# Kernel tuning notes

Hardware: AMD Instinct MI355X
Metric: run time of the kernel (lower is better)

Reference implementation:

```python
import jax, jax.numpy as jnp
import numpy as np

NH, NKV, HD, ROPE_DIMS, ROPE_BASE = 16, 4, 128, 64, 10000.0


def _rms_norm(x):
    eps = jnp.asarray(jnp.finfo(x.dtype).eps, x.dtype)
    return x * jax.lax.rsqrt(jnp.mean(x * x, axis=-1, keepdims=True) + eps)


def _apply_rope_partial(x, cos, sin):
    # x: [B, H, T, hd]; cos/sin: [T, rope_dims//2]
    h = ROPE_DIMS // 2
    xa, xb, xp = x[..., :h], x[..., h:ROPE_DIMS], x[..., ROPE_DIMS:]
    c, s = cos[None, None], sin[None, None]
    rot = jnp.concatenate([xa * c - xb * s, xa * s + xb * c], axis=-1)
    return jnp.concatenate([rot, xp], axis=-1)


def setup_inputs() -> dict:
    key = jax.random.key(0)
    ks = jax.random.split(key, 7)
    B, T, D = 2, 2048, 2048
    kv_dim = NKV * HD
    sc = lambda n: 1.0 / np.sqrt(n)
    return {
        "x": jax.random.normal(ks[0], (B, T, D), jnp.float32),
        "ve_embed": jax.random.normal(ks[1], (B, T, kv_dim), jnp.float32),
        "Wq": jax.random.normal(ks[2], (D, D), jnp.float32) * sc(D),
        "Wk": jax.random.normal(ks[3], (kv_dim, D), jnp.float32) * sc(D),
        "Wv": jax.random.normal(ks[4], (kv_dim, D), jnp.float32) * sc(D),
        "Wproj": jax.random.normal(ks[5], (D, D), jnp.float32) * sc(D),
        "q_gain": jnp.full((NH,), 12.0, jnp.float32)
        + 0.01 * jax.random.normal(ks[6], (NH,), jnp.float32),
    }


def reference(x, ve_embed, Wq, Wk, Wv, Wproj, q_gain):
    B, T, D = x.shape
    g = NH // NKV  # GQA group size

    # QKV projections -> [B, H, T, hd]
    q = (x @ Wq.T).reshape(B, T, NH, HD).transpose(0, 2, 1, 3)
    k = (x @ Wk.T).reshape(B, T, NKV, HD).transpose(0, 2, 1, 3)
    v = (x @ Wv.T).reshape(B, T, NKV, HD).transpose(0, 2, 1, 3)

    q, k = _rms_norm(q), _rms_norm(k)

    # partial RoPE (frequencies built over full hd, first rope_dims//2 used)
    inv_freq = 1.0 / ROPE_BASE ** (jnp.arange(0, HD, 2, dtype=jnp.float32) / HD)
    f = jnp.arange(T, dtype=jnp.float32)[:, None] * inv_freq[None, :]  # [T, hd//2]
    cos, sin = jnp.cos(f)[:, : ROPE_DIMS // 2], jnp.sin(f)[:, : ROPE_DIMS // 2]
    q = _apply_rope_partial(q, cos, sin)
    k = _apply_rope_partial(k, cos, sin)

    q = q * q_gain[None, :, None, None]
    v = v + ve_embed.reshape(B, T, NKV, HD).transpose(0, 2, 1, 3)

    # GQA causal attention: q grouped as [B, nkv, g, T, hd]
    qg = q.reshape(B, NKV, g, T, HD)
    scale = 1.0 / np.sqrt(HD)
    scores = jnp.einsum("bkgtd,bksd->bkgts", qg, k) * scale
    causal = jnp.tril(jnp.ones((T, T), bool))
    scores = jnp.where(causal[None, None, None], scores, -jnp.inf)
    p = jax.nn.softmax(scores, axis=-1)
    y = jnp.einsum("bkgts,bksd->bkgtd", p, v)  # [B, nkv, g, T, hd]

    y = y.reshape(B, NH, T, HD).transpose(0, 2, 1, 3).reshape(B, T, D)
    return y @ Wproj.T
```

## Files before the change

kernel.cpp:

```cpp
#include <hip/hip_runtime.h>
#include <hip/hip_bf16.h>
#include <cstdint>
#include <cstddef>


typedef _Float16 f16_t;
typedef f16_t f16x8 __attribute__((ext_vector_type(8)));
typedef float f32x4 __attribute__((ext_vector_type(4)));

#define MFMA16F(a, b, c) __builtin_amdgcn_mfma_f32_16x16x32_f16((a), (b), (c), 0, 0, 0)
#define SBAR()   __builtin_amdgcn_s_barrier()
#define SCHED0() __builtin_amdgcn_sched_barrier(0)
#define LGKM0()  asm volatile("s_waitcnt lgkmcnt(0)" ::: "memory")

__device__ __forceinline__ void gload16(const f16_t* g, f16_t* l) {
  auto lds_ptr = reinterpret_cast<__attribute__((address_space(3))) unsigned int*>(
      reinterpret_cast<uintptr_t>(l));
  auto g_ptr = reinterpret_cast<const __attribute__((address_space(1))) unsigned int*>(
      reinterpret_cast<uintptr_t>(g));
  __builtin_amdgcn_global_load_lds(g_ptr, lds_ptr, 16, 0, 0);
}

__global__ void k_cast_f16(const float* __restrict__ in, f16_t* __restrict__ o, long n) {
  long i = ((long)blockIdx.x * blockDim.x + threadIdx.x) * 4;
  const long step = (long)gridDim.x * blockDim.x * 4;
  for (; i < n; i += step) {
    const float4 v = *reinterpret_cast<const float4*>(in + i);
    f16_t r[4] = {(f16_t)v.x, (f16_t)v.y, (f16_t)v.z, (f16_t)v.w};
    *reinterpret_cast<uint64_t*>(o + i) = *reinterpret_cast<const uint64_t*>(r);
  }
}

__global__ void k_cast_wqkv(const float* __restrict__ Wq, const float* __restrict__ Wk,
                            const float* __restrict__ Wv, f16_t* __restrict__ wf) {
  long i = ((long)blockIdx.x * blockDim.x + threadIdx.x) * 4;
  const long step = (long)gridDim.x * blockDim.x * 4;
  for (; i < (long)3072 * 2048; i += step) {
    const long row = i >> 11, col = i & 2047;
    const float* src = (row < 2048) ? (Wq + (size_t)row * 2048)
                     : (row < 2560) ? (Wk + (size_t)(row - 2048) * 2048)
                                    : (Wv + (size_t)(row - 2560) * 2048);
    const float4 v = *reinterpret_cast<const float4*>(src + col);
    f16_t r[4] = {(f16_t)v.x, (f16_t)v.y, (f16_t)v.z, (f16_t)v.w};
    *reinterpret_cast<uint64_t*>(wf + row * 2048 + col) = *reinterpret_cast<const uint64_t*>(r);
  }
}

__global__ void k_rope_tab(float* __restrict__ ctab, float* __restrict__ stab) {
  const int idx = blockIdx.x * blockDim.x + threadIdx.x;
  if (idx >= 2048 * 32) return;
  const int t = idx >> 5, i = idx & 31;
  const float freq = exp2f(-(float)i * 0.2076205059304601f);
  const float f = (float)t * freq;
  ctab[idx] = cosf(f);
  stab[idx] = sinf(f);
}

__global__ __launch_bounds__(256) void k_vtrans(
    const f16_t* __restrict__ vn, f16_t* __restrict__ vt)
{
  __shared__ __align__(16) f16_t lsT[64 * 136];
  const int t0 = blockIdx.x * 64;
  const int bk = blockIdx.y;
  const f16_t* src = vn + ((size_t)bk * 2048 + t0) * 128;
  f16_t* dst = vt + (size_t)bk * 128 * 2048;
  const int tid = threadIdx.x;
#pragma unroll
  for (int it = 0; it < 4; ++it) {
    const int cch = tid + it * 256;
    const int r = cch >> 4, c = cch & 15;
    *reinterpret_cast<f16x8*>(&lsT[r * 136 + c * 8]) =
        *reinterpret_cast<const f16x8*>(src + (size_t)r * 128 + c * 8);
  }
  __syncthreads();
#pragma unroll
  for (int it = 0; it < 4; ++it) {
    const int u = tid + it * 256;
    const int d = u >> 3, c8 = u & 7;
    f16_t vals[8];
#pragma unroll
    for (int j = 0; j < 8; ++j) vals[j] = lsT[(c8 * 8 + j) * 136 + d];
    *reinterpret_cast<f16x8*>(dst + (size_t)d * 2048 + t0 + c8 * 8) =
        *reinterpret_cast<const f16x8*>(vals);
  }
}

template <int NBU, typename OutT>
__global__ __launch_bounds__(1024, 1) void k_gemmQ(
    const f16_t* __restrict__ A, const f16_t* __restrict__ Bm,
    OutT* __restrict__ C, int M, int N, int K, int lda, int ldb)
{
  __shared__ __align__(16) f16_t lds[2][(4 + NBU) * 4096];
  const int tid = threadIdx.x;
  const int l = tid & 63, w = tid >> 6;
  const int lrow = l & 15, lk = l >> 4;
  const int wm = w >> 2, wn = w & 3;

  const int nwg = gridDim.x * gridDim.y;
  int lin = blockIdx.y * gridDim.x + blockIdx.x;
  lin = (lin & 7) * (nwg >> 3) + (lin >> 3);
  const int m0 = (lin / gridDim.x) * 256, n0 = (lin % gridDim.x) * (64 * NBU);

  const bool stager = (tid < 512);
  const int srow = tid >> 3;
  const int scol = ((tid & 7) ^ (srow & 7)) << 3;
  const f16_t* gP[4 + NBU];
#pragma unroll
  for (int u = 0; u < 4; ++u) gP[u] = A + (size_t)(m0 + u * 64 + srow) * lda + scol;
#pragma unroll
  for (int u = 0; u < NBU; ++u) gP[4 + u] = Bm + (size_t)(n0 + u * 64 + srow) * ldb + scol;

  auto stageAll = [&](int buf, int k0) {
#pragma unroll
    for (int u = 0; u < 4 + NBU; ++u)
      gload16(gP[u] + k0, &lds[buf][u * 4096 + tid * 8]);
  };
  auto rdA = [&](int buf, int mf, int ks) -> f16x8 {
    const int row = wm * 64 + mf * 16 + lrow;
    const int slot = ((ks << 2) | lk) ^ (row & 7);
    return *reinterpret_cast<const f16x8*>(&lds[buf][row * 64 + slot * 8]);
  };
  auto rdB = [&](int buf, int nf, int ks) -> f16x8 {
    const int row = wn * (16 * NBU) + nf * 16 + lrow;
    const int slot = ((ks << 2) | lk) ^ (row & 7);
    return *reinterpret_cast<const f16x8*>(&lds[buf][16384 + row * 64 + slot * 8]);
  };

  f32x4 acc[4][NBU] = {};
  const int nkt = K >> 6;

  if (stager) {
    stageAll(0, 0);
    stageAll(1, nkt > 1 ? 64 : 0);
  }
  if constexpr (NBU == 3) { asm volatile("s_waitcnt vmcnt(7)" ::: "memory"); }
  else                    { asm volatile("s_waitcnt vmcnt(6)" ::: "memory"); }
  SCHED0();
  SBAR(); SCHED0();

  f16x8 aA[4][2], bB[NBU][2];
  for (int kt = 0; kt < nkt; ++kt) {
    const int b = kt & 1;
    const int kn2 = (kt + 2 < nkt ? kt + 2 : nkt - 1) << 6;

#pragma unroll
    for (int mf = 0; mf < 4; ++mf) { aA[mf][0] = rdA(b, mf, 0); aA[mf][1] = rdA(b, mf, 1); }
#pragma unroll
    for (int nf = 0; nf < NBU; ++nf) { bB[nf][0] = rdB(b, nf, 0); bB[nf][1] = rdB(b, nf, 1); }
    __builtin_amdgcn_s_setprio(1);
#pragma unroll
    for (int mf = 0; mf < 2; ++mf)
#pragma unroll
      for (int nf = 0; nf < NBU; ++nf)
#pragma unroll
        for (int ks = 0; ks < 2; ++ks)
          acc[mf][nf] = MFMA16F(aA[mf][ks], bB[nf][ks], acc[mf][nf]);
    __builtin_amdgcn_s_setprio(0);
    LGKM0(); SCHED0();
    SBAR(); SCHED0();

    if (stager) stageAll(b, kn2);
    if constexpr (NBU == 3) { asm volatile("s_waitcnt vmcnt(7)" ::: "memory"); }
    else                    { asm volatile("s_waitcnt vmcnt(6)" ::: "memory"); }
    SCHED0();
    __builtin_amdgcn_s_setprio(1);
#pragma unroll
    for (int mf = 2; mf < 4; ++mf)
#pragma unroll
      for (int nf = 0; nf < NBU; ++nf)
#pragma unroll
        for (int ks = 0; ks < 2; ++ks)
          acc[mf][nf] = MFMA16F(aA[mf][ks], bB[nf][ks], acc[mf][nf]);
    __builtin_amdgcn_s_setprio(0);
    SBAR(); SCHED0();
  }

#pragma unroll
  for (int mf = 0; mf < 4; ++mf) {
    const int row = m0 + wm * 64 + mf * 16 + lk * 4;
#pragma unroll
    for (int nf = 0; nf < NBU; ++nf) {
      const int col = n0 + wn * (16 * NBU) + nf * 16 + lrow;
#pragma unroll
      for (int rg = 0; rg < 4; ++rg)
        C[(size_t)(row + rg) * N + col] = (OutT)acc[mf][nf][rg];
    }
  }
  (void)M;
}

__global__ __launch_bounds__(256) void k_qkv_epi(
    const f16_t* __restrict__ qkv, const float* __restrict__ ve,
    const float* __restrict__ qgain,
    const float* __restrict__ ctab, const float* __restrict__ stab,
    f16_t* __restrict__ qn, f16_t* __restrict__ kn, f16_t* __restrict__ vn)
{
  const int blk = blockIdx.x;
  const int b = blk >> 11, t = blk & 2047;
  const int w = threadIdx.x >> 6, l = threadIdx.x & 63;
  const int i32 = l & 31;
  const float c = ctab[t * 32 + i32], s = stab[t * 32 + i32];
  const float EPS = 1.1920929e-07f;
  constexpr float SCALE_L2E = 0.088388347648318447f * 1.4426950408889634f;

#pragma unroll
  for (int it = 0; it < 4; ++it) {
    const int h = w + it * 4;
    const f16_t* row = qkv + (size_t)blk * 3072 + h * 128;
    float x0 = (float)row[l], x1 = (float)row[l + 64];
    float ss = x0 * x0 + x1 * x1;
#pragma unroll
    for (int off = 32; off; off >>= 1) ss += __shfl_xor(ss, off);
    const float rn = rsqrtf(ss * (1.0f / 128.0f) + EPS);
    x0 *= rn; x1 *= rn;
    const float p = __shfl_xor(x0, 32);
    float xr = (l < 32) ? (x0 * c - p * s) : (p * s + x0 * c);
    const float g = qgain[h] * SCALE_L2E;
    xr *= g; x1 *= g;
    f16_t* orow = qn + (((size_t)(b * 16 + h)) * 2048 + t) * 128;
    orow[l] = (f16_t)xr;
    orow[l + 64] = (f16_t)x1;
  }
  {
    const f16_t* row = qkv + (size_t)blk * 3072 + 2048 + w * 128;
    float x0 = (float)row[l], x1 = (float)row[l + 64];
    float ss = x0 * x0 + x1 * x1;
#pragma unroll
    for (int off = 32; off; off >>= 1) ss += __shfl_xor(ss, off);
    const float rn = rsqrtf(ss * (1.0f / 128.0f) + EPS);
    x0 *= rn; x1 *= rn;
    const float p = __shfl_xor(x0, 32);
    const float xr = (l < 32) ? (x0 * c - p * s) : (p * s + x0 * c);
    f16_t* orow = kn + (((size_t)(b * 4 + w)) * 2048 + t) * 128;
    orow[l] = (f16_t)xr;
    orow[l + 64] = (f16_t)x1;
  }
  {
    const f16_t* row = qkv + (size_t)blk * 3072 + 2560 + w * 128;
    const float* verow = ve + (size_t)blk * 512 + w * 128;
    f16_t* orow = vn + (((size_t)(b * 4 + w)) * 2048 + t) * 128;
    orow[l] = (f16_t)((float)row[l] + verow[l]);
    orow[l + 64] = (f16_t)((float)row[l + 64] + verow[l + 64]);
  }
}

__global__ __launch_bounds__(256, 3) void k_attn(
    const f16_t* __restrict__ qn, const f16_t* __restrict__ kn,
    const f16_t* __restrict__ vt, f16_t* __restrict__ y)
{
  __shared__ __align__(16) f16_t lsK[64 * 136];
  __shared__ __align__(16) f16_t lsV[128 * 72];
  __shared__ __align__(16) f16_t lsPb[4][16 * 72];
  const int qt = 31 - (int)blockIdx.y;
  const int bh = blockIdx.x;
  const int b = bh >> 4, h = bh & 15, kvh = h >> 2;
  const int tid = threadIdx.x, w = tid >> 6, l = tid & 63;
  const int lrow = l & 15, lk = l >> 4;
  const int qbase = qt * 64 + w * 16;
  constexpr float NEG = -1e30f;
  f16_t* lsP = lsPb[w];

  const f16_t* qp = qn + ((size_t)(b * 16 + h) * 2048) * 128;
  f16x8 aQ[4];
#pragma unroll
  for (int kf = 0; kf < 4; ++kf)
    aQ[kf] = *reinterpret_cast<const f16x8*>(
        qp + (size_t)(qbase + lrow) * 128 + kf * 32 + lk * 8);

  const f16_t* kp = kn + ((size_t)(b * 4 + kvh) * 2048) * 128;
  const f16_t* vtp = vt + (size_t)(b * 4 + kvh) * 128 * 2048;

  f32x4 o[8] = {};
  float mst[4], lst[4];
#pragma unroll
  for (int rg = 0; rg < 4; ++rg) { mst[rg] = NEG; lst[rg] = 0.f; }

  f16x8 kreg[4], vreg[4];
  auto loadKV = [&](int t0) {
#pragma unroll
    for (int it = 0; it < 4; ++it) {
      const int cch = tid + it * 256;
      kreg[it] = *reinterpret_cast<const f16x8*>(
          kp + (size_t)(t0 + (cch >> 4)) * 128 + (cch & 15) * 8);
      vreg[it] = *reinterpret_cast<const f16x8*>(
          vtp + (size_t)(cch >> 3) * 2048 + t0 + (cch & 7) * 8);
    }
  };
  loadKV(0);

  const int ntiles = qt + 1;
  for (int tt = 0; tt < ntiles; ++tt) {
    __syncthreads();
#pragma unroll
    for (int it = 0; it < 4; ++it) {
      const int cch = tid + it * 256;
      const int r = cch >> 4, dg = cch & 15;
      *reinterpret_cast<f16x8*>(&lsK[r * 136 + dg * 8]) = kreg[it];
      const int d = cch >> 3, c8 = cch & 7;
      *reinterpret_cast<f16x8*>(&lsV[d * 72 + ((c8 ^ ((d >> 3) & 7)) << 3)]) = vreg[it];
    }
    if (tt + 1 < ntiles) loadKV((tt + 1) * 64);
    __syncthreads();

    f32x4 sacc[4] = {};
#pragma unroll
    for (int cf = 0; cf < 4; ++cf) {
      const int krow = cf * 16 + lrow;
#pragma unroll
      for (int kf = 0; kf < 4; ++kf) {
        const f16x8 bK = *reinterpret_cast<const f16x8*>(
            &lsK[krow * 136 + kf * 32 + lk * 8]);
        sacc[cf] = MFMA16F(aQ[kf], bK, sacc[cf]);
      }
    }

    if (tt == qt) {
#pragma unroll
      for (int rg = 0; rg < 4; ++rg) {
        const int qi = w * 16 + lk * 4 + rg;
#pragma unroll
        for (int cf = 0; cf < 4; ++cf)
          if (cf * 16 + lrow > qi) sacc[cf][rg] = NEG;
      }
    }
    float pmax[4];
#pragma unroll
    for (int rg = 0; rg < 4; ++rg) {
      float mx = fmaxf(fmaxf(sacc[0][rg], sacc[1][rg]),
                       fmaxf(sacc[2][rg], sacc[3][rg]));
      mx = fmaxf(mx, __shfl_xor(mx, 1));
      mx = fmaxf(mx, __shfl_xor(mx, 2));
      mx = fmaxf(mx, __shfl_xor(mx, 4));
      mx = fmaxf(mx, __shfl_xor(mx, 8));
      pmax[rg] = mx;
    }
    const bool grow = (pmax[0] > mst[0] + 8.f) | (pmax[1] > mst[1] + 8.f) |
                      (pmax[2] > mst[2] + 8.f) | (pmax[3] > mst[3] + 8.f);
    if (__any(grow)) {
#pragma unroll
      for (int rg = 0; rg < 4; ++rg) {
        const float mnew = fmaxf(mst[rg], pmax[rg]);
        const float alpha = exp2f(mst[rg] - mnew);
        mst[rg] = mnew;
        lst[rg] *= alpha;
#pragma unroll
        for (int df = 0; df < 8; ++df) o[df][rg] *= alpha;
      }
    }
#pragma unroll
    for (int rg = 0; rg < 4; ++rg) {
      float rsum = 0.f;
#pragma unroll
      for (int cf = 0; cf < 4; ++cf) {
        const float p = exp2f(sacc[cf][rg] - mst[rg]);
        sacc[cf][rg] = p;
        rsum += p;
      }
      rsum += __shfl_xor(rsum, 1);
      rsum += __shfl_xor(rsum, 2);
      rsum += __shfl_xor(rsum, 4);
      rsum += __shfl_xor(rsum, 8);
      lst[rg] += rsum;
    }

#pragma unroll
    for (int cf = 0; cf < 4; ++cf)
#pragma unroll
      for (int rg = 0; rg < 4; ++rg)
        lsP[(lk * 4 + rg) * 72 + cf * 16 + lrow] = (f16_t)sacc[cf][rg];
#pragma unroll
    for (int k2 = 0; k2 < 2; ++k2) {
      const f16x8 aP = *reinterpret_cast<const f16x8*>(
          &lsP[lrow * 72 + k2 * 32 + lk * 8]);
#pragma unroll
      for (int df = 0; df < 8; ++df) {
        const int row = df * 16 + lrow;
        const int colb = (k2 * 32 + lk * 8) ^ (((row >> 3) & 7) << 3);
        const f16x8 bV = *reinterpret_cast<const f16x8*>(&lsV[row * 72 + colb]);
        o[df] = MFMA16F(aP, bV, o[df]);
      }
    }
  }

#pragma unroll
  for (int rg = 0; rg < 4; ++rg) {
    const float inv = 1.0f / lst[rg];
    const int qi = qbase + lk * 4 + rg;
    const size_t rowoff = ((size_t)(b * 2048 + qi)) * 2048 + h * 128;
#pragma unroll
    for (int df = 0; df < 8; ++df)
      y[rowoff + df * 16 + lrow] = (f16_t)(o[df][rg] * inv);
  }
}

extern "C" void kernel_launch(void* const* d_in, const int* in_sizes, int n_in,
                              void* d_out, int out_size, void* d_ws, size_t ws_size,
                              hipStream_t stream) {
  const float* x  = (const float*)d_in[0];
  const float* ve = (const float*)d_in[1];
  const float* Wq = (const float*)d_in[2];
  const float* Wk = (const float*)d_in[3];
  const float* Wv = (const float*)d_in[4];
  const float* Wp = (const float*)d_in[5];
  const float* qg = (const float*)d_in[6];
  float* out = (float*)d_out;

  char* ws = (char*)d_ws;
  size_t off = 0;
  auto alloc = [&](size_t bytes) -> char* {
    char* p = ws + off;
    off += (bytes + 255) & ~(size_t)255;
    return p;
  };

  f16_t* xf    = (f16_t*)alloc((size_t)4096 * 2048 * 2);
  f16_t* wqkvf = (f16_t*)alloc((size_t)3072 * 2048 * 2);
  f16_t* wpf   = (f16_t*)alloc((size_t)2048 * 2048 * 2);
  f16_t* qkvf  = (f16_t*)alloc((size_t)4096 * 3072 * 2);
  f16_t* kn    = (f16_t*)alloc((size_t)2 * 4 * 2048 * 128 * 2);
  f16_t* vn    = (f16_t*)alloc((size_t)2 * 4 * 2048 * 128 * 2);
  f16_t* vt    = (f16_t*)alloc((size_t)2 * 4 * 128 * 2048 * 2);
  float* ctab  = (float*)alloc((size_t)2048 * 32 * 4);
  float* stab  = (float*)alloc((size_t)2048 * 32 * 4);
  f16_t* qn    = xf;
  f16_t* yb    = qkvf;
  (void)ws_size; (void)in_sizes; (void)n_in; (void)out_size;

  k_cast_f16<<<1024, 256, 0, stream>>>(x, xf, (long)4096 * 2048);
  k_cast_wqkv<<<1536, 256, 0, stream>>>(Wq, Wk, Wv, wqkvf);
  k_cast_f16<<<1024, 256, 0, stream>>>(Wp, wpf, (long)2048 * 2048);
  k_rope_tab<<<256, 256, 0, stream>>>(ctab, stab);

  k_gemmQ<3, f16_t><<<dim3(16, 16), 1024, 0, stream>>>(
      xf, wqkvf, qkvf, 4096, 3072, 2048, 2048, 2048);

  k_qkv_epi<<<4096, 256, 0, stream>>>(qkvf, ve, qg, ctab, stab, qn, kn, vn);

  k_vtrans<<<dim3(32, 8), 256, 0, stream>>>(vn, vt);

  k_attn<<<dim3(32, 32), 256, 0, stream>>>(qn, kn, vt, yb);

  k_gemmQ<2, float><<<dim3(16, 16), 1024, 0, stream>>>(
      yb, wpf, out, 4096, 2048, 2048, 2048, 2048);
}
```

Measured before the change: 215.2 us.

## Split long causal attention query tiles into two KV halves with combine kernel

```diff
diff --git a/kernel.cpp b/kernel.cpp
--- a/kernel.cpp
+++ b/kernel.cpp
@@ -246,12 +246,23 @@
 
 __global__ __launch_bounds__(256, 3) void k_attn(
     const f16_t* __restrict__ qn, const f16_t* __restrict__ kn,
-    const f16_t* __restrict__ vt, f16_t* __restrict__ y)
+    const f16_t* __restrict__ vt, f16_t* __restrict__ y,
+    f16_t* __restrict__ po, float* __restrict__ pm, float* __restrict__ pl)
 {
   __shared__ __align__(16) f16_t lsK[64 * 136];
   __shared__ __align__(16) f16_t lsV[128 * 72];
   __shared__ __align__(16) f16_t lsPb[4][16 * 72];
-  const int qt = 31 - (int)blockIdx.y;
+  const int j = blockIdx.y;
+  int qt, sp, tstart, tcnt;
+  bool split;
+  if (j < 32) {
+    qt = 31 - (j >> 1); sp = j & 1; split = true;
+    const int tot = qt + 1, c0 = (tot + 1) >> 1;
+    tstart = sp ? c0 : 0;
+    tcnt = sp ? tot - c0 : c0;
+  } else {
+    qt = 47 - j; sp = 0; split = false; tstart = 0; tcnt = qt + 1;
+  }
   const int bh = blockIdx.x;
   const int b = bh >> 4, h = bh & 15, kvh = h >> 2;
   const int tid = threadIdx.x, w = tid >> 6, l = tid & 63;
@@ -286,10 +297,10 @@
           vtp + (size_t)(cch >> 3) * 2048 + t0 + (cch & 7) * 8);
     }
   };
-  loadKV(0);
-
-  const int ntiles = qt + 1;
-  for (int tt = 0; tt < ntiles; ++tt) {
+  loadKV(tstart * 64);
+
+  for (int ti = 0; ti < tcnt; ++ti) {
+    const int tt = tstart + ti;
     __syncthreads();
 #pragma unroll
     for (int it = 0; it < 4; ++it) {
@@ -299,7 +310,7 @@
       const int d = cch >> 3, c8 = cch & 7;
       *reinterpret_cast<f16x8*>(&lsV[d * 72 + ((c8 ^ ((d >> 3) & 7)) << 3)]) = vreg[it];
     }
-    if (tt + 1 < ntiles) loadKV((tt + 1) * 64);
+    if (ti + 1 < tcnt) loadKV((tt + 1) * 64);
     __syncthreads();
 
     f32x4 sacc[4] = {};
@@ -356,10 +367,6 @@
         sacc[cf][rg] = p;
         rsum += p;
       }
-      rsum += __shfl_xor(rsum, 1);
-      rsum += __shfl_xor(rsum, 2);
-      rsum += __shfl_xor(rsum, 4);
-      rsum += __shfl_xor(rsum, 8);
       lst[rg] += rsum;
     }
 
@@ -384,12 +391,66 @@
 
 #pragma unroll
   for (int rg = 0; rg < 4; ++rg) {
-    const float inv = 1.0f / lst[rg];
-    const int qi = qbase + lk * 4 + rg;
-    const size_t rowoff = ((size_t)(b * 2048 + qi)) * 2048 + h * 128;
-#pragma unroll
-    for (int df = 0; df < 8; ++df)
-      y[rowoff + df * 16 + lrow] = (f16_t)(o[df][rg] * inv);
+    float s = lst[rg];
+    s += __shfl_xor(s, 1);
+    s += __shfl_xor(s, 2);
+    s += __shfl_xor(s, 4);
+    s += __shfl_xor(s, 8);
+    lst[rg] = s;
+  }
+
+  if (!split) {
+#pragma unroll
+    for (int rg = 0; rg < 4; ++rg) {
+      const float inv = 1.0f / lst[rg];
+      const int qi = qbase + lk * 4 + rg;
+      const size_t rowoff = ((size_t)(b * 2048 + qi)) * 2048 + h * 128;
+#pragma unroll
+      for (int df = 0; df < 8; ++df)
+        y[rowoff + df * 16 + lrow] = (f16_t)(o[df][rg] * inv);
+    }
+  } else {
+#pragma unroll
+    for (int rg = 0; rg < 4; ++rg) {
+      const int qi = qbase + lk * 4 + rg;
+      const size_t base = (((size_t)(sp * 2 + b) * 16 + h) * 1024 + (qi - 1024));
+      f16_t* prow = po + base * 128;
+#pragma unroll
+      for (int df = 0; df < 8; ++df)
+        prow[df * 16 + lrow] = (f16_t)o[df][rg];
+      if (lrow == 0) { pm[base] = mst[rg]; pl[base] = lst[rg]; }
+    }
+  }
+}
+
+__global__ __launch_bounds__(256) void k_combine(
+    const f16_t* __restrict__ po, const float* __restrict__ pm,
+    const float* __restrict__ pl, f16_t* __restrict__ y)
+{
+  const int bh = blockIdx.x;
+  const int b = bh >> 4, h = bh & 15;
+  const int tid = threadIdx.x;
+  const int r = blockIdx.y * 32 + (tid >> 3);
+  const int d0 = (tid & 7) * 16;
+  const size_t base1 = (((size_t)(0 * 2 + b) * 16 + h) * 1024 + r);
+  const size_t base2 = (((size_t)(1 * 2 + b) * 16 + h) * 1024 + r);
+  const float m1 = pm[base1], m2 = pm[base2];
+  const float l1 = pl[base1], l2 = pl[base2];
+  const float m = fmaxf(m1, m2);
+  const float f1 = exp2f(m1 - m), f2 = exp2f(m2 - m);
+  const float inv = 1.0f / (f1 * l1 + f2 * l2);
+  const f16_t* o1 = po + base1 * 128 + d0;
+  const f16_t* o2 = po + base2 * 128 + d0;
+  f16_t* yr = y + ((size_t)(b * 2048 + 1024 + r)) * 2048 + h * 128 + d0;
+#pragma unroll
+  for (int v = 0; v < 2; ++v) {
+    const f16x8 a = *reinterpret_cast<const f16x8*>(o1 + v * 8);
+    const f16x8 c = *reinterpret_cast<const f16x8*>(o2 + v * 8);
+    f16_t outv[8];
+#pragma unroll
+    for (int jj = 0; jj < 8; ++jj)
+      outv[jj] = (f16_t)((f1 * (float)a[jj] + f2 * (float)c[jj]) * inv);
+    *reinterpret_cast<f16x8*>(yr + v * 8) = *reinterpret_cast<const f16x8*>(outv);
   }
 }
 
@@ -420,6 +481,9 @@
   f16_t* kn    = (f16_t*)alloc((size_t)2 * 4 * 2048 * 128 * 2);
   f16_t* vn    = (f16_t*)alloc((size_t)2 * 4 * 2048 * 128 * 2);
   f16_t* vt    = (f16_t*)alloc((size_t)2 * 4 * 128 * 2048 * 2);
+  f16_t* po    = (f16_t*)alloc((size_t)2 * 2 * 16 * 1024 * 128 * 2);
+  float* pm    = (float*)alloc((size_t)2 * 2 * 16 * 1024 * 4);
+  float* pl    = (float*)alloc((size_t)2 * 2 * 16 * 1024 * 4);
   float* ctab  = (float*)alloc((size_t)2048 * 32 * 4);
   float* stab  = (float*)alloc((size_t)2048 * 32 * 4);
   f16_t* qn    = xf;
@@ -438,7 +502,9 @@
 
   k_vtrans<<<dim3(32, 8), 256, 0, stream>>>(vn, vt);
 
-  k_attn<<<dim3(32, 32), 256, 0, stream>>>(qn, kn, vt, yb);
+  k_attn<<<dim3(32, 48), 256, 0, stream>>>(qn, kn, vt, yb, po, pm, pl);
+
+  k_combine<<<dim3(32, 32), 256, 0, stream>>>(po, pm, pl, yb);
 
   k_gemmQ<2, float><<<dim3(16, 16), 1024, 0, stream>>>(
       yb, wpf, out, 4096, 2048, 2048, 2048, 2048);
```

Measured after the change: 218.1 us. About the same (+1.4%).

## Transpose QK^T MFMA so each lane owns one query row; XOR-swizzle unpadded LDS

Applied to the files above, without the earlier changes.

```diff
diff --git a/kernel.cpp b/kernel.cpp
--- a/kernel.cpp
+++ b/kernel.cpp
@@ -5,6 +5,7 @@
 
 
 typedef _Float16 f16_t;
+typedef f16_t f16x4 __attribute__((ext_vector_type(4)));
 typedef f16_t f16x8 __attribute__((ext_vector_type(8)));
 typedef float f32x4 __attribute__((ext_vector_type(4)));
 
@@ -244,13 +245,13 @@
   }
 }
 
-__global__ __launch_bounds__(256, 3) void k_attn(
+__global__ __launch_bounds__(256, 4) void k_attn(
     const f16_t* __restrict__ qn, const f16_t* __restrict__ kn,
     const f16_t* __restrict__ vt, f16_t* __restrict__ y)
 {
-  __shared__ __align__(16) f16_t lsK[64 * 136];
-  __shared__ __align__(16) f16_t lsV[128 * 72];
-  __shared__ __align__(16) f16_t lsPb[4][16 * 72];
+  __shared__ __align__(16) f16_t lsK[64 * 128];
+  __shared__ __align__(16) f16_t lsV[128 * 64];
+  __shared__ __align__(16) f16_t lsPb[4][16 * 64];
   const int qt = 31 - (int)blockIdx.y;
   const int bh = blockIdx.x;
   const int b = bh >> 4, h = bh & 15, kvh = h >> 2;
@@ -271,9 +272,8 @@
   const f16_t* vtp = vt + (size_t)(b * 4 + kvh) * 128 * 2048;
 
   f32x4 o[8] = {};
-  float mst[4], lst[4];
-#pragma unroll
-  for (int rg = 0; rg < 4; ++rg) { mst[rg] = NEG; lst[rg] = 0.f; }
+  float mst = NEG;
+  float lst = 0.f;
 
   f16x8 kreg[4], vreg[4];
   auto loadKV = [&](int t0) {
@@ -295,9 +295,9 @@
     for (int it = 0; it < 4; ++it) {
       const int cch = tid + it * 256;
       const int r = cch >> 4, dg = cch & 15;
-      *reinterpret_cast<f16x8*>(&lsK[r * 136 + dg * 8]) = kreg[it];
+      *reinterpret_cast<f16x8*>(&lsK[r * 128 + ((dg ^ (r & 7)) << 3)]) = kreg[it];
       const int d = cch >> 3, c8 = cch & 7;
-      *reinterpret_cast<f16x8*>(&lsV[d * 72 + ((c8 ^ ((d >> 3) & 7)) << 3)]) = vreg[it];
+      *reinterpret_cast<f16x8*>(&lsV[d * 64 + ((c8 ^ ((d >> 3) & 7)) << 3)]) = vreg[it];
     }
     if (tt + 1 < ntiles) loadKV((tt + 1) * 64);
     __syncthreads();
@@ -308,83 +308,81 @@
       const int krow = cf * 16 + lrow;
 #pragma unroll
       for (int kf = 0; kf < 4; ++kf) {
-        const f16x8 bK = *reinterpret_cast<const f16x8*>(
-            &lsK[krow * 136 + kf * 32 + lk * 8]);
-        sacc[cf] = MFMA16F(aQ[kf], bK, sacc[cf]);
+        const f16x8 aK = *reinterpret_cast<const f16x8*>(
+            &lsK[krow * 128 + ((((kf << 2) | lk) ^ (krow & 7)) << 3)]);
+        sacc[cf] = MFMA16F(aK, aQ[kf], sacc[cf]);
       }
     }
 
     if (tt == qt) {
+      const int qin = w * 16 + lrow;
+#pragma unroll
+      for (int cf = 0; cf < 4; ++cf)
+#pragma unroll
+        for (int rg = 0; rg < 4; ++rg)
+          if (cf * 16 + lk * 4 + rg > qin) sacc[cf][rg] = NEG;
+    }
+
+    float mx = NEG;
+#pragma unroll
+    for (int cf = 0; cf < 4; ++cf)
+      mx = fmaxf(mx, fmaxf(fmaxf(sacc[cf][0], sacc[cf][1]),
+                           fmaxf(sacc[cf][2], sacc[cf][3])));
+    if (__any(mx > mst + 8.f)) {
+      float rmx = mx;
+      rmx = fmaxf(rmx, __shfl_xor(rmx, 16));
+      rmx = fmaxf(rmx, __shfl_xor(rmx, 32));
+      const float mnew = fmaxf(mst, rmx);
+      const float alpha = exp2f(mst - mnew);
+      mst = mnew;
+      lst *= alpha;
 #pragma unroll
       for (int rg = 0; rg < 4; ++rg) {
-        const int qi = w * 16 + lk * 4 + rg;
-#pragma unroll
-        for (int cf = 0; cf < 4; ++cf)
-          if (cf * 16 + lrow > qi) sacc[cf][rg] = NEG;
+        const float arow = __shfl(alpha, lk * 4 + rg);
+#pragma unroll
+        for (int df = 0; df < 8; ++df) o[df][rg] *= arow;
       }
     }
-    float pmax[4];
-#pragma unroll
-    for (int rg = 0; rg < 4; ++rg) {
-      float mx = fmaxf(fmaxf(sacc[0][rg], sacc[1][rg]),
-                       fmaxf(sacc[2][rg], sacc[3][rg]));
-      mx = fmaxf(mx, __shfl_xor(mx, 1));
-      mx = fmaxf(mx, __shfl_xor(mx, 2));
-      mx = fmaxf(mx, __shfl_xor(mx, 4));
-      mx = fmaxf(mx, __shfl_xor(mx, 8));
-      pmax[rg] = mx;
-    }
-    const bool grow = (pmax[0] > mst[0] + 8.f) | (pmax[1] > mst[1] + 8.f) |
-                      (pmax[2] > mst[2] + 8.f) | (pmax[3] > mst[3] + 8.f);
-    if (__any(grow)) {
+#pragma unroll
+    for (int cf = 0; cf < 4; ++cf) {
 #pragma unroll
       for (int rg = 0; rg < 4; ++rg) {
-        const float mnew = fmaxf(mst[rg], pmax[rg]);
-        const float alpha = exp2f(mst[rg] - mnew);
-        mst[rg] = mnew;
-        lst[rg] *= alpha;
-#pragma unroll
-        for (int df = 0; df < 8; ++df) o[df][rg] *= alpha;
+        const float p = exp2f(sacc[cf][rg] - mst);
+        sacc[cf][rg] = p;
+        lst += p;
       }
     }
-#pragma unroll
-    for (int rg = 0; rg < 4; ++rg) {
-      float rsum = 0.f;
-#pragma unroll
-      for (int cf = 0; cf < 4; ++cf) {
-        const float p = exp2f(sacc[cf][rg] - mst[rg]);
-        sacc[cf][rg] = p;
-        rsum += p;
-      }
-      rsum += __shfl_xor(rsum, 1);
-      rsum += __shfl_xor(rsum, 2);
-      rsum += __shfl_xor(rsum, 4);
-      rsum += __shfl_xor(rsum, 8);
-      lst[rg] += rsum;
-    }
-
-#pragma unroll
-    for (int cf = 0; cf < 4; ++cf)
-#pragma unroll
-      for (int rg = 0; rg < 4; ++rg)
-        lsP[(lk * 4 + rg) * 72 + cf * 16 + lrow] = (f16_t)sacc[cf][rg];
+
+#pragma unroll
+    for (int cf = 0; cf < 4; ++cf) {
+      f16x4 pk;
+#pragma unroll
+      for (int rg = 0; rg < 4; ++rg) pk[rg] = (f16_t)sacc[cf][rg];
+      const int slot8 = cf * 2 + (lk >> 1);
+      *reinterpret_cast<f16x4*>(
+          &lsP[lrow * 64 + ((slot8 ^ (lrow & 7)) << 3) + (lk & 1) * 4]) = pk;
+    }
 #pragma unroll
     for (int k2 = 0; k2 < 2; ++k2) {
       const f16x8 aP = *reinterpret_cast<const f16x8*>(
-          &lsP[lrow * 72 + k2 * 32 + lk * 8]);
+          &lsP[lrow * 64 + ((((k2 << 2) | lk) ^ (lrow & 7)) << 3)]);
 #pragma unroll
       for (int df = 0; df < 8; ++df) {
         const int row = df * 16 + lrow;
-        const int colb = (k2 * 32 + lk * 8) ^ (((row >> 3) & 7) << 3);
-        const f16x8 bV = *reinterpret_cast<const f16x8*>(&lsV[row * 72 + colb]);
+        const f16x8 bV = *reinterpret_cast<const f16x8*>(
+            &lsV[row * 64 + ((((k2 << 2) | lk) ^ ((row >> 3) & 7)) << 3)]);
         o[df] = MFMA16F(aP, bV, o[df]);
       }
     }
   }
 
+  lst += __shfl_xor(lst, 16);
+  lst += __shfl_xor(lst, 32);
+
 #pragma unroll
   for (int rg = 0; rg < 4; ++rg) {
-    const float inv = 1.0f / lst[rg];
+    const float lrow_sum = __shfl(lst, lk * 4 + rg);
+    const float inv = 1.0f / lrow_sum;
     const int qi = qbase + lk * 4 + rg;
     const size_t rowoff = ((size_t)(b * 2048 + qi)) * 2048 + h * 128;
 #pragma unroll
```

After: 344.6 us. +60.1%, slower.
